# Kernel optimization log

Measured on AMD Instinct MI355X. Metric: run time of the kernel, lower is better.

The kernel has to match this reference:

```python
import jax, jax.numpy as jnp
import numpy as np

B, S, D = 2, 2048, 512
M = 64            # meta_memory_dim
C = 16            # n_chunks
H = 8             # attention heads
WIN = 512         # sliding window size
N_LAYERS = 2      # n_hidden_layers of ResLinear
MAX_ALR = 0.01    # max_adaptive_lr
LR, WD, EPS = 1e-3, 1e-2, 1e-8  # AdamW hyperparams (first step from zero state)
T = M + S


def lmm_apply(ws, x):
    # ResLinear: bias-free residual MLP blocks, x <- x + silu(x W^T)
    for W in ws:
        x = x + jax.nn.silu(x @ W.T)
    return x


def chunkify(t, c):
    # [B, T, D] -> [B, L, C, D] with contiguous chunks on axis 2 (vmap in_dims=2)
    b, t_, d = t.shape
    return jnp.moveaxis(t.reshape(b, c, t_ // c, d), 1, 2)


def swa(x, wq, wk, wv, wo):
    # causal sliding-window multi-head attention
    b, t, d = x.shape
    hd = d // H
    q = (x @ wq.T).reshape(b, t, H, hd)
    k = (x @ wk.T).reshape(b, t, H, hd)
    v = (x @ wv.T).reshape(b, t, H, hd)
    scores = jnp.einsum('bqhd,bkhd->bhqk', q, k) / jnp.sqrt(jnp.float32(hd))
    i = jnp.arange(t)[:, None]
    j = jnp.arange(t)[None, :]
    mask = (j <= i) & (i - j < WIN)
    scores = jnp.where(mask, scores, jnp.finfo(scores.dtype).min)
    attn = jax.nn.softmax(scores, axis=-1)
    out = jnp.einsum('bhqk,bkhd->bqhd', attn, v).reshape(b, t, d)
    return out @ wo.T


def setup_inputs() -> dict:
    key = jax.random.key(0)
    ks = jax.random.split(key, 11)
    sc = 0.02
    return {
        'x': jax.random.normal(ks[0], (B, S, D), jnp.float32),
        'meta_memory': jax.random.normal(ks[1], (M, D), jnp.float32),
        'lmm_w': jax.random.normal(ks[2], (N_LAYERS, D, D), jnp.float32) * sc,
        'w_q': jax.random.normal(ks[3], (D, D), jnp.float32) * sc,
        'w_k': jax.random.normal(ks[4], (D, D), jnp.float32) * sc,
        'w_v': jax.random.normal(ks[5], (D, D), jnp.float32) * sc,
        'w_lr': jax.random.normal(ks[6], (1, D), jnp.float32) * sc,
        'swa_wq': jax.random.normal(ks[7], (D, D), jnp.float32) * sc,
        'swa_wk': jax.random.normal(ks[8], (D, D), jnp.float32) * sc,
        'swa_wv': jax.random.normal(ks[9], (D, D), jnp.float32) * sc,
        'swa_wo': jax.random.normal(ks[10], (D, D), jnp.float32) * sc,
    }


def reference(x, meta_memory, lmm_w, w_q, w_k, w_v, w_lr, swa_wq, swa_wk, swa_wv, swa_wo):
    # inject meta memory tokens
    meta = jnp.broadcast_to(meta_memory, (x.shape[0],) + meta_memory.shape)
    xm = jnp.concatenate([meta, x], axis=1)                   # [B, T, D]

    queries = xm @ w_q.T                                      # [B, T, D] (n_chunks=1)
    keys = chunkify(xm @ w_k.T, C)                            # [B, L, C, D]
    values = chunkify(xm @ w_v.T, C)                          # [B, L, C, D]
    alr = chunkify(jax.nn.sigmoid(xm @ w_lr.T) * MAX_ALR, C)  # [B, L, C, 1]

    def assoc_loss(ws, k, v, w):
        preds = lmm_apply(ws, k)                              # [B, L, D]
        loss = jnp.mean((preds - v) ** 2, axis=-1)            # [B, L]
        return jnp.sum(loss * w[..., 0])

    # per-chunk test-time gradients of the associative loss
    grads = jax.vmap(jax.grad(assoc_loss), in_axes=(None, 2, 2, 2))(lmm_w, keys, values, alr)
    g = grads.mean(axis=0)                                    # [N_LAYERS, D, D]

    # first AdamW step from zero optimizer state: m_hat=g, v_hat=g^2
    lmm_w_new = lmm_w * (1.0 - LR * WD) - LR * g / (jnp.sqrt(g * g) + EPS)

    retrieved = lmm_apply(lmm_w_new, queries)                 # [B, T, D]
    retrieved = swa(retrieved, swa_wq, swa_wk, swa_wv, swa_wo)
    return retrieved[:, M:, :]                                # drop meta tokens
```

## Files before the change

### kernel.cpp

```cpp
#include <hip/hip_runtime.h>
#include <hip/hip_bf16.h>

#define B_   2
#define S_   2048
#define D_   512
#define M_   64
#define T_   2112
#define BT_  4224
#define H_   8
#define WIN_ 512

typedef short s16x8 __attribute__((ext_vector_type(8)));
typedef float f32x4 __attribute__((ext_vector_type(4)));
typedef unsigned short ushort_t;

__device__ __forceinline__ float siluf(float x) {
    float s = 1.0f / (1.0f + expf(-x));
    return x * s;
}
__device__ __forceinline__ float dsiluf(float x) {
    float s = 1.0f / (1.0f + expf(-x));
    return s * (1.0f + x * (1.0f - s));
}
__device__ __forceinline__ float bf2f(ushort_t u) {
    union { float f; unsigned int i; } x; x.i = ((unsigned int)u) << 16; return x.f;
}
__device__ __forceinline__ ushort_t f2bf(float f) {
    union { float f; unsigned int i; } x; x.f = f;
    unsigned int r = x.i + 0x7FFFu + ((x.i >> 16) & 1u);
    return (ushort_t)(r >> 16);
}
__device__ __forceinline__ void pack8(ushort_t* dst, const float* v) {
    ushort_t tmp[8];
#pragma unroll
    for (int i = 0; i < 8; ++i) tmp[i] = f2bf(v[i]);
    *(int4*)dst = *(const int4*)tmp;
}

__global__ void build_xm_kernel(const float* __restrict__ x, const float* __restrict__ meta,
                                ushort_t* __restrict__ xmb) {
    int idx = blockIdx.x * 256 + threadIdx.x;
    int seg = idx & 63;
    int row = idx >> 6;
    int b   = row / T_;
    int t   = row - b * T_;
    const float* src;
    if (t < M_) src = meta + (size_t)t * 512 + seg * 8;
    else        src = x + ((size_t)b * S_ + (t - M_)) * 512 + seg * 8;
    float v[8];
    *(float4*)&v[0] = *(const float4*)src;
    *(float4*)&v[4] = *(const float4*)(src + 4);
    pack8(xmb + (size_t)row * 512 + seg * 8, v);
}

struct W9 { const float* s[9]; ushort_t* d[9]; };
__global__ void cvt_w_kernel(W9 p) {
    int w = blockIdx.y;
    int idx = blockIdx.x * 256 + threadIdx.x;
    const float* src = p.s[w] + (size_t)idx * 8;
    float v[8];
    *(float4*)&v[0] = *(const float4*)src;
    *(float4*)&v[4] = *(const float4*)(src + 4);
    pack8(p.d[w] + (size_t)idx * 8, v);
}
__global__ void cvt_wT_kernel(const float* __restrict__ src, ushort_t* __restrict__ dst) {
    __shared__ float t[32][33];
    int tid = threadIdx.x;
    int tr = tid >> 3, tc = (tid & 7) * 4;
    int r0 = blockIdx.y * 32, c0 = blockIdx.x * 32;
    *(float4*)&t[tr][tc] = *(const float4*)&src[(size_t)(r0 + tr) * 512 + c0 + tc];
    __syncthreads();
    ushort_t o[4];
#pragma unroll
    for (int i = 0; i < 4; ++i) o[i] = f2bf(t[tc + i][tr]);
    *(ushort2*)&dst[(size_t)(c0 + tr) * 512 + r0 + tc] = *(ushort2*)&o[0];
    *(ushort2*)&dst[(size_t)(c0 + tr) * 512 + r0 + tc + 2] = *(ushort2*)&o[2];
}

__global__ void alr_kernel(const ushort_t* __restrict__ xmb, const float* __restrict__ wlr,
                           float* __restrict__ alr) {
    int r = blockIdx.x * 4 + (threadIdx.x >> 6);
    int lane = threadIdx.x & 63;
    const ushort_t* row = xmb + (size_t)r * D_;
    float s = 0.f;
#pragma unroll
    for (int k = 0; k < 8; ++k) s = fmaf(bf2f(row[lane + k * 64]), wlr[lane + k * 64], s);
#pragma unroll
    for (int off = 32; off >= 1; off >>= 1) s += __shfl_xor(s, off, 64);
    if (lane == 0) alr[r] = 0.01f / (1.0f + expf(-s));
}

template<int MODE>
__global__ __launch_bounds__(256)
void mgemm(const ushort_t* __restrict__ A, const ushort_t* __restrict__ Bt,
           float* __restrict__ F0, float* __restrict__ F1,
           ushort_t* __restrict__ U0, ushort_t* __restrict__ U1, ushort_t* __restrict__ U2,
           const float* __restrict__ alrp) {
    __shared__ ushort_t As[64 * 64];
    __shared__ ushort_t Bs[64 * 64];
    int tid = threadIdx.x;
    int m0 = blockIdx.x * 64, n0 = blockIdx.y * 64;
    int srow = tid >> 2;
    int sseg = (tid & 3) << 1;
    int wid = tid >> 6;
    int lane = tid & 63;
    int wm = (wid & 1) << 5;
    int wn = (wid >> 1) << 5;
    int fr = lane & 15;
    int fq = lane >> 4;
    f32x4 acc[2][2] = {};
    for (int k0 = 0; k0 < 512; k0 += 64) {
        const ushort_t* ga = A  + (size_t)(m0 + srow) * 512 + k0 + sseg * 8;
        const ushort_t* gb = Bt + (size_t)(n0 + srow) * 512 + k0 + sseg * 8;
        int4 av0 = *(const int4*)ga;
        int4 av1 = *(const int4*)(ga + 8);
        int4 bv0 = *(const int4*)gb;
        int4 bv1 = *(const int4*)(gb + 8);
        __syncthreads();
        int sw = srow & 7;
        *(int4*)&As[srow * 64 + ((sseg    ) ^ sw) * 8] = av0;
        *(int4*)&As[srow * 64 + ((sseg + 1) ^ sw) * 8] = av1;
        *(int4*)&Bs[srow * 64 + ((sseg    ) ^ sw) * 8] = bv0;
        *(int4*)&Bs[srow * 64 + ((sseg + 1) ^ sw) * 8] = bv1;
        __syncthreads();
#pragma unroll
        for (int ks = 0; ks < 2; ++ks) {
            int seg = fq + ks * 4;
            int rA0 = wm + fr,      rA1 = wm + 16 + fr;
            int rB0 = wn + fr,      rB1 = wn + 16 + fr;
            s16x8 a0 = *(const s16x8*)&As[rA0 * 64 + (seg ^ (rA0 & 7)) * 8];
            s16x8 a1 = *(const s16x8*)&As[rA1 * 64 + (seg ^ (rA1 & 7)) * 8];
            s16x8 b0 = *(const s16x8*)&Bs[rB0 * 64 + (seg ^ (rB0 & 7)) * 8];
            s16x8 b1 = *(const s16x8*)&Bs[rB1 * 64 + (seg ^ (rB1 & 7)) * 8];
            acc[0][0] = __builtin_amdgcn_mfma_f32_16x16x32_bf16(a0, b0, acc[0][0], 0, 0, 0);
            acc[0][1] = __builtin_amdgcn_mfma_f32_16x16x32_bf16(a0, b1, acc[0][1], 0, 0, 0);
            acc[1][0] = __builtin_amdgcn_mfma_f32_16x16x32_bf16(a1, b0, acc[1][0], 0, 0, 0);
            acc[1][1] = __builtin_amdgcn_mfma_f32_16x16x32_bf16(a1, b1, acc[1][1], 0, 0, 0);
        }
    }
#pragma unroll
    for (int i = 0; i < 2; ++i) {
        int row0 = m0 + wm + i * 16 + fq * 4;
        float c4[4];
        if (MODE == 2) {
#pragma unroll
            for (int r = 0; r < 4; ++r) c4[r] = (2.0f / 512.0f) * alrp[row0 + r];
        }
#pragma unroll
        for (int j = 0; j < 2; ++j) {
            int col = n0 + wn + j * 16 + fr;
            if (MODE == 0 || MODE == 5) {
                int sg = col >> 9;
                int cl = col & 511;
                if (MODE == 0) {
                    ushort_t* dst = (sg == 0) ? U0 : ((sg == 1) ? U1 : U2);
#pragma unroll
                    for (int r = 0; r < 4; ++r)
                        dst[(size_t)(row0 + r) * 512 + cl] = f2bf(acc[i][j][r]);
                } else {
                    if (sg == 0) {
#pragma unroll
                        for (int r = 0; r < 4; ++r)
                            U0[(size_t)(row0 + r) * 512 + cl] = f2bf(acc[i][j][r]);
                    } else if (sg == 1) {
#pragma unroll
                        for (int r = 0; r < 4; ++r)
                            U1[(size_t)(row0 + r) * 512 + cl] = f2bf(acc[i][j][r]);
                    } else {
                        int bb = row0 / T_;
                        int t0 = row0 - bb * T_;
                        ushort_t t4[4];
#pragma unroll
                        for (int r = 0; r < 4; ++r) t4[r] = f2bf(acc[i][j][r]);
                        *(uint2*)&U2[((size_t)(bb * 512) + cl) * T_ + t0] = *(uint2*)t4;
                    }
                }
            } else {
#pragma unroll
                for (int r = 0; r < 4; ++r) {
                    size_t off = (size_t)(row0 + r) * 512 + col;
                    float v = acc[i][j][r];
                    if (MODE == 1) {
                        F1[off] = v;
                        float h = bf2f(U1[off]) + siluf(v);
                        F0[off] = h;
                        U0[off] = f2bf(h);
                    } else if (MODE == 2) {
                        float z = v;
                        float s = 1.f / (1.f + expf(-z));
                        float d = c4[r] * (F0[off] + z * s - bf2f(U1[off]));
                        F1[off] = d;
                        U0[off] = f2bf(d * (s * (1.f + z * (1.f - s))));
                    } else if (MODE == 3) {
                        float g = F0[off] + v;
                        U0[off] = f2bf(g * dsiluf(F1[off]));
                    } else if (MODE == 4) {
                        U0[off] = f2bf(bf2f(U1[off]) + siluf(v));
                    } else if (MODE == 6) {
                        int row = row0 + r;
                        int bb = row / T_;
                        int t = row - bb * T_;
                        if (t >= M_) F0[((size_t)bb * S_ + (t - M_)) * 512 + col] = v;
                    }
                }
            }
        }
    }
}

__global__ __launch_bounds__(256)
void gemm_tn_bf(const ushort_t* __restrict__ A, const ushort_t* __restrict__ Bm,
                float* __restrict__ Cpart) {
    __shared__ ushort_t At[64 * 64];
    __shared__ ushort_t Bt[64 * 64];
    int tid = threadIdx.x;
    int m0 = blockIdx.x * 64, n0 = blockIdx.y * 64;
    int kbase = blockIdx.z * 704;
    int wave = tid >> 6, lane = tid & 63;
    int fr = lane & 15, fq = lane >> 4;
    int wm = (wave & 1) << 5, wn = (wave >> 1) << 5;
    int tok = tid & 63, cs0 = tid >> 6;
    f32x4 acc[2][2] = {};
    for (int kt = 0; kt < 11; ++kt) {
        int t0 = kbase + kt * 64;
        int4 av[2], bv[2];
#pragma unroll
        for (int p = 0; p < 2; ++p) {
            int cs = cs0 + p * 4;
            av[p] = *(const int4*)&A[(size_t)(t0 + tok) * 512 + m0 + cs * 8];
            bv[p] = *(const int4*)&Bm[(size_t)(t0 + tok) * 512 + n0 + cs * 8];
        }
        __syncthreads();
#pragma unroll
        for (int p = 0; p < 2; ++p) {
            int cs = cs0 + p * 4;
            const ushort_t* au = (const ushort_t*)&av[p];
            const ushort_t* bu = (const ushort_t*)&bv[p];
#pragma unroll
            for (int j = 0; j < 8; ++j) {
                int row = cs * 8 + j;
                At[row * 64 + (((tok >> 3) ^ j) << 3) + (tok & 7)] = au[j];
                Bt[row * 64 + (((tok >> 3) ^ j) << 3) + (tok & 7)] = bu[j];
            }
        }
        __syncthreads();
#pragma unroll
        for (int ks = 0; ks < 2; ++ks) {
            int seg = ks * 4 + fq;
            s16x8 a0 = *(const s16x8*)&At[(wm + fr) * 64      + ((seg ^ (fr & 7)) << 3)];
            s16x8 a1 = *(const s16x8*)&At[(wm + 16 + fr) * 64 + ((seg ^ (fr & 7)) << 3)];
            s16x8 b0 = *(const s16x8*)&Bt[(wn + fr) * 64      + ((seg ^ (fr & 7)) << 3)];
            s16x8 b1 = *(const s16x8*)&Bt[(wn + 16 + fr) * 64 + ((seg ^ (fr & 7)) << 3)];
            acc[0][0] = __builtin_amdgcn_mfma_f32_16x16x32_bf16(a0, b0, acc[0][0], 0, 0, 0);
            acc[0][1] = __builtin_amdgcn_mfma_f32_16x16x32_bf16(a0, b1, acc[0][1], 0, 0, 0);
            acc[1][0] = __builtin_amdgcn_mfma_f32_16x16x32_bf16(a1, b0, acc[1][0], 0, 0, 0);
            acc[1][1] = __builtin_amdgcn_mfma_f32_16x16x32_bf16(a1, b1, acc[1][1], 0, 0, 0);
        }
    }
    float* C = Cpart + (size_t)blockIdx.z * 262144;
#pragma unroll
    for (int i = 0; i < 2; ++i)
#pragma unroll
        for (int j = 0; j < 2; ++j)
#pragma unroll
            for (int r = 0; r < 4; ++r)
                C[(size_t)(m0 + wm + i * 16 + fq * 4 + r) * 512 + n0 + wn + j * 16 + fr] =
                    acc[i][j][r];
}

__global__ void adam_kernel(const float* __restrict__ W, const float* __restrict__ dWp,
                            ushort_t* __restrict__ Wnb) {
    int idx = blockIdx.x * 256 + threadIdx.x;
    int layer = idx >> 18;
    int i = idx & 262143;
    const float* base = dWp + (size_t)layer * 6 * 262144 + i;
    float g = 0.f;
#pragma unroll
    for (int z = 0; z < 6; ++z) g += base[(size_t)z * 262144];
    g *= (1.0f / 16.0f);
    float w = W[idx];
    float o = w * (1.0f - 1e-5f) - 1e-3f * g / (fabsf(g) + 1e-8f);
    Wnb[idx] = f2bf(o);
}

__global__ __launch_bounds__(256)
void swa_mfma(const ushort_t* __restrict__ qh, const ushort_t* __restrict__ kh,
              const ushort_t* __restrict__ vhT, ushort_t* __restrict__ ao) {
    __shared__ ushort_t Qs[64 * 64];
    __shared__ ushort_t Ks[64 * 64];
    __shared__ ushort_t Vs[64 * 64];
    __shared__ ushort_t Pw[4][16 * 72];
    int qt = 32 - (int)blockIdx.x;
    int hh = blockIdx.y;
    int b  = blockIdx.z;
    int tid = threadIdx.x;
    int wave = tid >> 6, lane = tid & 63;
    int fr = lane & 15, fq = lane >> 4;
    int tok = tid & 63, cs0 = tid >> 6;

    {
        const ushort_t* src = qh + ((size_t)(b * T_ + qt * 64 + tok)) * 512 + hh * 64;
#pragma unroll
        for (int p = 0; p < 2; ++p) {
            int seg = cs0 + p * 4;
            *(int4*)&Qs[tok * 64 + ((seg ^ (tok & 7)) << 3)] = *(const int4*)(src + seg * 8);
        }
    }
    __syncthreads();
    s16x8 qf0 = *(const s16x8*)&Qs[(wave * 16 + fr) * 64 + (((0 + fq) ^ (fr & 7)) << 3)];
    s16x8 qf1 = *(const s16x8*)&Qs[(wave * 16 + fr) * 64 + (((4 + fq) ^ (fr & 7)) << 3)];

    int i_q = qt * 64 + wave * 16 + fr;
    float m_i = -1e30f, l_i = 0.f;
    f32x4 o[4] = {};
    int jstart = qt * 64 - (WIN_ - 1);
    if (jstart < 0) jstart = 0;
    jstart &= ~63;
    for (int jb = jstart; jb <= qt * 64; jb += 64) {
        __syncthreads();
        {
            const ushort_t* ksrc = kh + ((size_t)(b * T_ + jb + tok)) * 512 + hh * 64;
            const ushort_t* vsrc = vhT + ((size_t)(b * 512 + hh * 64 + tok)) * T_ + jb;
#pragma unroll
            for (int p = 0; p < 2; ++p) {
                int seg = cs0 + p * 4;
                *(int4*)&Ks[tok * 64 + ((seg ^ (tok & 7)) << 3)] = *(const int4*)(ksrc + seg * 8);
                *(int4*)&Vs[tok * 64 + ((seg ^ (tok & 7)) << 3)] = *(const int4*)(vsrc + seg * 8);
            }
        }
        __syncthreads();
        f32x4 sa[4] = {};
#pragma unroll
        for (int kf = 0; kf < 4; ++kf) {
            int krow = kf * 16 + fr;
            s16x8 a0 = *(const s16x8*)&Ks[krow * 64 + (((0 + fq) ^ (fr & 7)) << 3)];
            s16x8 a1 = *(const s16x8*)&Ks[krow * 64 + (((4 + fq) ^ (fr & 7)) << 3)];
            sa[kf] = __builtin_amdgcn_mfma_f32_16x16x32_bf16(a0, qf0, sa[kf], 0, 0, 0);
            sa[kf] = __builtin_amdgcn_mfma_f32_16x16x32_bf16(a1, qf1, sa[kf], 0, 0, 0);
        }
        float sv[16];
        float tmax = -1e30f;
#pragma unroll
        for (int kf = 0; kf < 4; ++kf)
#pragma unroll
            for (int r = 0; r < 4; ++r) {
                int j2 = jb + kf * 16 + fq * 4 + r;
                bool valid = (j2 <= i_q) && (i_q - j2 < WIN_);
                float v = valid ? sa[kf][r] * 0.125f : -1e30f;
                sv[kf * 4 + r] = v;
                tmax = fmaxf(tmax, v);
            }
        tmax = fmaxf(tmax, __shfl_xor(tmax, 16));
        tmax = fmaxf(tmax, __shfl_xor(tmax, 32));
        float mn = fmaxf(m_i, tmax);
        float alpha = __expf(m_i - mn);
        m_i = mn;
        float psum = 0.f;
#pragma unroll
        for (int kf = 0; kf < 4; ++kf)
#pragma unroll
            for (int r = 0; r < 4; ++r) {
                float v = sv[kf * 4 + r];
                float p = (v > -1e29f) ? __expf(v - mn) : 0.f;
                ushort_t pb = f2bf(p);
                psum += bf2f(pb);
                Pw[wave][fr * 72 + kf * 16 + fq * 4 + r] = pb;
            }
        psum += __shfl_xor(psum, 16);
        psum += __shfl_xor(psum, 32);
        l_i = l_i * alpha + psum;
        float a0s = __shfl(alpha, fq * 4 + 0);
        float a1s = __shfl(alpha, fq * 4 + 1);
        float a2s = __shfl(alpha, fq * 4 + 2);
        float a3s = __shfl(alpha, fq * 4 + 3);
#pragma unroll
        for (int nf = 0; nf < 4; ++nf) {
            o[nf][0] *= a0s; o[nf][1] *= a1s; o[nf][2] *= a2s; o[nf][3] *= a3s;
        }
#pragma unroll
        for (int ks = 0; ks < 2; ++ks) {
            s16x8 pa = *(const s16x8*)&Pw[wave][fr * 72 + ks * 32 + fq * 8];
#pragma unroll
            for (int nf = 0; nf < 4; ++nf) {
                int vrow = nf * 16 + fr;
                s16x8 bv = *(const s16x8*)&Vs[vrow * 64 + (((ks * 4 + fq) ^ (fr & 7)) << 3)];
                o[nf] = __builtin_amdgcn_mfma_f32_16x16x32_bf16(pa, bv, o[nf], 0, 0, 0);
            }
        }
    }
    float linv = 1.0f / l_i;
    float l0 = __shfl(linv, fq * 4 + 0);
    float l1 = __shfl(linv, fq * 4 + 1);
    float l2 = __shfl(linv, fq * 4 + 2);
    float l3 = __shfl(linv, fq * 4 + 3);
#pragma unroll
    for (int nf = 0; nf < 4; ++nf) {
        int col = hh * 64 + nf * 16 + fr;
        size_t row0 = (size_t)(b * T_) + qt * 64 + wave * 16 + fq * 4;
        ao[(row0 + 0) * 512 + col] = f2bf(o[nf][0] * l0);
        ao[(row0 + 1) * 512 + col] = f2bf(o[nf][1] * l1);
        ao[(row0 + 2) * 512 + col] = f2bf(o[nf][2] * l2);
        ao[(row0 + 3) * 512 + col] = f2bf(o[nf][3] * l3);
    }
}

extern "C" void kernel_launch(void* const* d_in, const int* in_sizes, int n_in,
                              void* d_out, int out_size, void* d_ws, size_t ws_size,
                              hipStream_t stream) {
    (void)in_sizes; (void)n_in; (void)out_size; (void)ws_size;
    const float* x      = (const float*)d_in[0];
    const float* meta   = (const float*)d_in[1];
    const float* lmm_w  = (const float*)d_in[2];
    const float* w_q    = (const float*)d_in[3];
    const float* w_k    = (const float*)d_in[4];
    const float* w_v    = (const float*)d_in[5];
    const float* w_lr   = (const float*)d_in[6];
    const float* swa_wq = (const float*)d_in[7];
    const float* swa_wk = (const float*)d_in[8];
    const float* swa_wv = (const float*)d_in[9];
    const float* swa_wo = (const float*)d_in[10];
    float* out = (float*)d_out;
    float* ws  = (float*)d_ws;

    const size_t BTD = (size_t)BT_ * D_;
    float* b4 = ws + 0 * BTD;
    float* b5 = ws + 1 * BTD;
    float* b7 = ws + 2 * BTD;
    float* alr = ws + 3 * BTD;
    float* dWp = alr + BT_;
    ushort_t* xb = (ushort_t*)(dWp + 12 * 262144);
    ushort_t* xm_bf  = xb + 0 * BTD;
    ushort_t* qq_bf  = xb + 1 * BTD;
    ushort_t* kk_bf  = xb + 2 * BTD;
    ushort_t* vv_bf  = xb + 3 * BTD;
    ushort_t* h1_bf  = xb + 4 * BTD;
    ushort_t* dz1_bf = xb + 5 * BTD;
    ushort_t* r_bf   = xm_bf;
    ushort_t* h1q_bf = kk_bf;
    ushort_t* qh_bf  = qq_bf;
    ushort_t* kh_bf  = dz1_bf;
    ushort_t* dz0_bf = vv_bf;
    ushort_t* ao_bf  = vv_bf;
    ushort_t* vhT    = h1_bf;
    ushort_t* wbf = xb + 6 * BTD;
    ushort_t* wq_bf  = wbf + 0 * 262144;
    ushort_t* l0_bf  = wbf + 3 * 262144;
    ushort_t* l1_bf  = wbf + 4 * 262144;
    ushort_t* sq_bf  = wbf + 5 * 262144;
    ushort_t* wo_bf  = wbf + 8 * 262144;
    ushort_t* l1t_bf = wbf + 9 * 262144;
    ushort_t* wn_bf  = wbf + 10 * 262144;

    dim3 blk(256);
    dim3 g8(1056);
    dim3 gg(66, 8);
    dim3 gq(66, 24);
    dim3 gtn(8, 8, 6);

    W9 wl;
    wl.s[0] = w_q;    wl.d[0] = wq_bf;
    wl.s[1] = w_k;    wl.d[1] = wbf + 1 * 262144;
    wl.s[2] = w_v;    wl.d[2] = wbf + 2 * 262144;
    wl.s[3] = lmm_w;  wl.d[3] = l0_bf;
    wl.s[4] = lmm_w + 262144; wl.d[4] = l1_bf;
    wl.s[5] = swa_wq; wl.d[5] = sq_bf;
    wl.s[6] = swa_wk; wl.d[6] = wbf + 6 * 262144;
    wl.s[7] = swa_wv; wl.d[7] = wbf + 7 * 262144;
    wl.s[8] = swa_wo; wl.d[8] = wo_bf;

    cvt_w_kernel<<<dim3(128, 9), blk, 0, stream>>>(wl);
    cvt_wT_kernel<<<dim3(16, 16), blk, 0, stream>>>(lmm_w + 262144, l1t_bf);
    build_xm_kernel<<<g8, blk, 0, stream>>>(x, meta, xm_bf);
    alr_kernel<<<dim3(1056), blk, 0, stream>>>(xm_bf, w_lr, alr);
    mgemm<0><<<gq, blk, 0, stream>>>(xm_bf, wq_bf, nullptr, nullptr, qq_bf, kk_bf, vv_bf, nullptr);
    mgemm<1><<<gg, blk, 0, stream>>>(kk_bf, l0_bf, b5, b4, h1_bf, kk_bf, nullptr, nullptr);
    mgemm<2><<<gg, blk, 0, stream>>>(h1_bf, l1_bf, b5, b7, dz1_bf, vv_bf, nullptr, alr);
    mgemm<3><<<gg, blk, 0, stream>>>(dz1_bf, l1t_bf, b7, b4, dz0_bf, nullptr, nullptr, nullptr);
    gemm_tn_bf<<<gtn, blk, 0, stream>>>(dz1_bf, h1_bf, dWp + 6 * 262144);
    gemm_tn_bf<<<gtn, blk, 0, stream>>>(dz0_bf, kk_bf, dWp);
    adam_kernel<<<dim3(2048), blk, 0, stream>>>(lmm_w, dWp, wn_bf);
    mgemm<4><<<gg, blk, 0, stream>>>(qq_bf, wn_bf, nullptr, nullptr, h1q_bf, qq_bf, nullptr, nullptr);
    mgemm<4><<<gg, blk, 0, stream>>>(h1q_bf, wn_bf + 262144, nullptr, nullptr, r_bf, h1q_bf, nullptr, nullptr);
    mgemm<5><<<gq, blk, 0, stream>>>(r_bf, sq_bf, nullptr, nullptr, qh_bf, kh_bf, vhT, nullptr);
    swa_mfma<<<dim3(33, 8, 2), blk, 0, stream>>>(qh_bf, kh_bf, vhT, ao_bf);
    mgemm<6><<<gg, blk, 0, stream>>>(ao_bf, wo_bf, out, nullptr, nullptr, nullptr, nullptr, nullptr);
}
```

Before: 246.6 us.

## Fuse prep kernels, register-prefetch GEMM tiles, emit transposed operands for dW GEMMs

Merges the weight conversion, transpose, xm build and alr kernels into one prep launch, with alr now computed from fp32 inputs. Adds register prefetch of the next K tile in mgemm, the dW GEMM and the sliding-window attention loop, so global loads overlap the MFMA work. The forward GEMM epilogues now also write token-major transposed copies, which lets the dW GEMM load contiguous rows instead of scattering elements into shared memory. Attention skips mask evaluation for fully valid tiles. In exchange it needs more workspace buffers, more epilogue stores and more register pressure.

```diff
diff --git a/kernel.cpp b/kernel.cpp
--- a/kernel.cpp
+++ b/kernel.cpp
@@ -37,64 +37,72 @@
     *(int4*)dst = *(const int4*)tmp;
 }
 
-__global__ void build_xm_kernel(const float* __restrict__ x, const float* __restrict__ meta,
-                                ushort_t* __restrict__ xmb) {
-    int idx = blockIdx.x * 256 + threadIdx.x;
-    int seg = idx & 63;
-    int row = idx >> 6;
-    int b   = row / T_;
-    int t   = row - b * T_;
-    const float* src;
-    if (t < M_) src = meta + (size_t)t * 512 + seg * 8;
-    else        src = x + ((size_t)b * S_ + (t - M_)) * 512 + seg * 8;
-    float v[8];
-    *(float4*)&v[0] = *(const float4*)src;
-    *(float4*)&v[4] = *(const float4*)(src + 4);
-    pack8(xmb + (size_t)row * 512 + seg * 8, v);
-}
-
-struct W9 { const float* s[9]; ushort_t* d[9]; };
-__global__ void cvt_w_kernel(W9 p) {
-    int w = blockIdx.y;
-    int idx = blockIdx.x * 256 + threadIdx.x;
-    const float* src = p.s[w] + (size_t)idx * 8;
-    float v[8];
-    *(float4*)&v[0] = *(const float4*)src;
-    *(float4*)&v[4] = *(const float4*)(src + 4);
-    pack8(p.d[w] + (size_t)idx * 8, v);
-}
-__global__ void cvt_wT_kernel(const float* __restrict__ src, ushort_t* __restrict__ dst) {
-    __shared__ float t[32][33];
+struct PrepArgs {
+    const float* wsrc[9]; ushort_t* wdst[9];
+    const float* l1src;   ushort_t* l1t;
+    const float* x; const float* meta; ushort_t* xm;
+    const float* wlr; float* alr;
+};
+__global__ __launch_bounds__(256)
+void prep_kernel(PrepArgs p) {
+    __shared__ float tbuf[32][33];
+    int bid = blockIdx.x;
     int tid = threadIdx.x;
-    int tr = tid >> 3, tc = (tid & 7) * 4;
-    int r0 = blockIdx.y * 32, c0 = blockIdx.x * 32;
-    *(float4*)&t[tr][tc] = *(const float4*)&src[(size_t)(r0 + tr) * 512 + c0 + tc];
-    __syncthreads();
-    ushort_t o[4];
-#pragma unroll
-    for (int i = 0; i < 4; ++i) o[i] = f2bf(t[tc + i][tr]);
-    *(ushort2*)&dst[(size_t)(c0 + tr) * 512 + r0 + tc] = *(ushort2*)&o[0];
-    *(ushort2*)&dst[(size_t)(c0 + tr) * 512 + r0 + tc + 2] = *(ushort2*)&o[2];
-}
-
-__global__ void alr_kernel(const ushort_t* __restrict__ xmb, const float* __restrict__ wlr,
-                           float* __restrict__ alr) {
-    int r = blockIdx.x * 4 + (threadIdx.x >> 6);
-    int lane = threadIdx.x & 63;
-    const ushort_t* row = xmb + (size_t)r * D_;
-    float s = 0.f;
-#pragma unroll
-    for (int k = 0; k < 8; ++k) s = fmaf(bf2f(row[lane + k * 64]), wlr[lane + k * 64], s);
-#pragma unroll
-    for (int off = 32; off >= 1; off >>= 1) s += __shfl_xor(s, off, 64);
-    if (lane == 0) alr[r] = 0.01f / (1.0f + expf(-s));
+    if (bid < 1152) {
+        int w = bid >> 7;
+        int idx = ((bid & 127) << 8) + tid;
+        const float* src = p.wsrc[w] + (size_t)idx * 8;
+        float v[8];
+        *(float4*)&v[0] = *(const float4*)src;
+        *(float4*)&v[4] = *(const float4*)(src + 4);
+        pack8(p.wdst[w] + (size_t)idx * 8, v);
+    } else if (bid < 1408) {
+        int wz = bid - 1152;
+        int bx = wz & 15, by = wz >> 4;
+        int tr = tid >> 3, tc = (tid & 7) * 4;
+        int r0 = by * 32, c0 = bx * 32;
+        *(float4*)&tbuf[tr][tc] = *(const float4*)&p.l1src[(size_t)(r0 + tr) * 512 + c0 + tc];
+        __syncthreads();
+        ushort_t o[4];
+#pragma unroll
+        for (int i = 0; i < 4; ++i) o[i] = f2bf(tbuf[tc + i][tr]);
+        *(ushort2*)&p.l1t[(size_t)(c0 + tr) * 512 + r0 + tc] = *(ushort2*)&o[0];
+        *(ushort2*)&p.l1t[(size_t)(c0 + tr) * 512 + r0 + tc + 2] = *(ushort2*)&o[2];
+    } else if (bid < 2464) {
+        int idx = (bid - 1408) * 256 + tid;
+        int seg = idx & 63;
+        int row = idx >> 6;
+        int b = row / T_;
+        int t = row - b * T_;
+        const float* src;
+        if (t < M_) src = p.meta + (size_t)t * 512 + seg * 8;
+        else        src = p.x + ((size_t)b * S_ + (t - M_)) * 512 + seg * 8;
+        float v[8];
+        *(float4*)&v[0] = *(const float4*)src;
+        *(float4*)&v[4] = *(const float4*)(src + 4);
+        pack8(p.xm + (size_t)row * 512 + seg * 8, v);
+    } else {
+        int r = (bid - 2464) * 4 + (tid >> 6);
+        int lane = tid & 63;
+        int b = r / T_;
+        int t = r - b * T_;
+        const float* row = (t < M_) ? (p.meta + (size_t)t * 512)
+                                    : (p.x + ((size_t)b * S_ + (t - M_)) * 512);
+        float s = 0.f;
+#pragma unroll
+        for (int k = 0; k < 8; ++k) s = fmaf(row[lane + k * 64], p.wlr[lane + k * 64], s);
+#pragma unroll
+        for (int off = 32; off >= 1; off >>= 1) s += __shfl_xor(s, off, 64);
+        if (lane == 0) p.alr[r] = 0.01f / (1.0f + expf(-s));
+    }
 }
 
 template<int MODE>
 __global__ __launch_bounds__(256)
 void mgemm(const ushort_t* __restrict__ A, const ushort_t* __restrict__ Bt,
            float* __restrict__ F0, float* __restrict__ F1,
-           ushort_t* __restrict__ U0, ushort_t* __restrict__ U1, ushort_t* __restrict__ U2,
+           ushort_t* __restrict__ U0, ushort_t* __restrict__ U1,
+           ushort_t* __restrict__ U2, ushort_t* __restrict__ U3,
            const float* __restrict__ alrp) {
     __shared__ ushort_t As[64 * 64];
     __shared__ ushort_t Bs[64 * 64];
@@ -108,21 +116,27 @@
     int wn = (wid >> 1) << 5;
     int fr = lane & 15;
     int fq = lane >> 4;
+    int sw = srow & 7;
+    const ushort_t* ga = A  + (size_t)(m0 + srow) * 512 + sseg * 8;
+    const ushort_t* gb = Bt + (size_t)(n0 + srow) * 512 + sseg * 8;
+    int4 av0 = *(const int4*)ga;
+    int4 av1 = *(const int4*)(ga + 8);
+    int4 bv0 = *(const int4*)gb;
+    int4 bv1 = *(const int4*)(gb + 8);
     f32x4 acc[2][2] = {};
     for (int k0 = 0; k0 < 512; k0 += 64) {
-        const ushort_t* ga = A  + (size_t)(m0 + srow) * 512 + k0 + sseg * 8;
-        const ushort_t* gb = Bt + (size_t)(n0 + srow) * 512 + k0 + sseg * 8;
-        int4 av0 = *(const int4*)ga;
-        int4 av1 = *(const int4*)(ga + 8);
-        int4 bv0 = *(const int4*)gb;
-        int4 bv1 = *(const int4*)(gb + 8);
-        __syncthreads();
-        int sw = srow & 7;
+        __syncthreads();
         *(int4*)&As[srow * 64 + ((sseg    ) ^ sw) * 8] = av0;
         *(int4*)&As[srow * 64 + ((sseg + 1) ^ sw) * 8] = av1;
         *(int4*)&Bs[srow * 64 + ((sseg    ) ^ sw) * 8] = bv0;
         *(int4*)&Bs[srow * 64 + ((sseg + 1) ^ sw) * 8] = bv1;
         __syncthreads();
+        if (k0 + 64 < 512) {
+            av0 = *(const int4*)(ga + k0 + 64);
+            av1 = *(const int4*)(ga + k0 + 72);
+            bv0 = *(const int4*)(gb + k0 + 64);
+            bv1 = *(const int4*)(gb + k0 + 72);
+        }
 #pragma unroll
         for (int ks = 0; ks < 2; ++ks) {
             int seg = fq + ks * 4;
@@ -149,59 +163,88 @@
 #pragma unroll
         for (int j = 0; j < 2; ++j) {
             int col = n0 + wn + j * 16 + fr;
-            if (MODE == 0 || MODE == 5) {
-                int sg = col >> 9;
-                int cl = col & 511;
-                if (MODE == 0) {
-                    ushort_t* dst = (sg == 0) ? U0 : ((sg == 1) ? U1 : U2);
-#pragma unroll
-                    for (int r = 0; r < 4; ++r)
-                        dst[(size_t)(row0 + r) * 512 + cl] = f2bf(acc[i][j][r]);
+            if (MODE == 0) {
+                int sg = col >> 9, cl = col & 511;
+                ushort_t t4[4];
+#pragma unroll
+                for (int r = 0; r < 4; ++r) t4[r] = f2bf(acc[i][j][r]);
+                if (sg == 0) {
+#pragma unroll
+                    for (int r = 0; r < 4; ++r) U0[(size_t)(row0 + r) * 512 + cl] = t4[r];
+                } else if (sg == 1) {
+#pragma unroll
+                    for (int r = 0; r < 4; ++r) U1[(size_t)(row0 + r) * 512 + cl] = t4[r];
+                    *(uint2*)&U2[(size_t)cl * BT_ + row0] = *(uint2*)t4;
                 } else {
-                    if (sg == 0) {
-#pragma unroll
-                        for (int r = 0; r < 4; ++r)
-                            U0[(size_t)(row0 + r) * 512 + cl] = f2bf(acc[i][j][r]);
-                    } else if (sg == 1) {
-#pragma unroll
-                        for (int r = 0; r < 4; ++r)
-                            U1[(size_t)(row0 + r) * 512 + cl] = f2bf(acc[i][j][r]);
-                    } else {
-                        int bb = row0 / T_;
-                        int t0 = row0 - bb * T_;
-                        ushort_t t4[4];
-#pragma unroll
-                        for (int r = 0; r < 4; ++r) t4[r] = f2bf(acc[i][j][r]);
-                        *(uint2*)&U2[((size_t)(bb * 512) + cl) * T_ + t0] = *(uint2*)t4;
-                    }
-                }
-            } else {
+#pragma unroll
+                    for (int r = 0; r < 4; ++r) U3[(size_t)(row0 + r) * 512 + cl] = t4[r];
+                }
+            } else if (MODE == 5) {
+                int sg = col >> 9, cl = col & 511;
+                ushort_t t4[4];
+#pragma unroll
+                for (int r = 0; r < 4; ++r) t4[r] = f2bf(acc[i][j][r]);
+                if (sg == 0) {
+#pragma unroll
+                    for (int r = 0; r < 4; ++r) U0[(size_t)(row0 + r) * 512 + cl] = t4[r];
+                } else if (sg == 1) {
+#pragma unroll
+                    for (int r = 0; r < 4; ++r) U1[(size_t)(row0 + r) * 512 + cl] = t4[r];
+                } else {
+                    int bb = row0 / T_;
+                    int t0 = row0 - bb * T_;
+                    *(uint2*)&U2[((size_t)(bb * 512) + cl) * T_ + t0] = *(uint2*)t4;
+                }
+            } else if (MODE == 1) {
+                ushort_t t4[4];
 #pragma unroll
                 for (int r = 0; r < 4; ++r) {
                     size_t off = (size_t)(row0 + r) * 512 + col;
-                    float v = acc[i][j][r];
-                    if (MODE == 1) {
-                        F1[off] = v;
-                        float h = bf2f(U1[off]) + siluf(v);
-                        F0[off] = h;
-                        U0[off] = f2bf(h);
-                    } else if (MODE == 2) {
-                        float z = v;
-                        float s = 1.f / (1.f + expf(-z));
-                        float d = c4[r] * (F0[off] + z * s - bf2f(U1[off]));
-                        F1[off] = d;
-                        U0[off] = f2bf(d * (s * (1.f + z * (1.f - s))));
-                    } else if (MODE == 3) {
-                        float g = F0[off] + v;
-                        U0[off] = f2bf(g * dsiluf(F1[off]));
-                    } else if (MODE == 4) {
-                        U0[off] = f2bf(bf2f(U1[off]) + siluf(v));
-                    } else if (MODE == 6) {
-                        int row = row0 + r;
-                        int bb = row / T_;
-                        int t = row - bb * T_;
-                        if (t >= M_) F0[((size_t)bb * S_ + (t - M_)) * 512 + col] = v;
-                    }
+                    float z = acc[i][j][r];
+                    F1[off] = z;
+                    float h = bf2f(U1[off]) + siluf(z);
+                    F0[off] = h;
+                    ushort_t hb = f2bf(h);
+                    U0[off] = hb;
+                    t4[r] = hb;
+                }
+                *(uint2*)&U2[(size_t)col * BT_ + row0] = *(uint2*)t4;
+            } else if (MODE == 2) {
+                ushort_t t4[4];
+#pragma unroll
+                for (int r = 0; r < 4; ++r) {
+                    size_t off = (size_t)(row0 + r) * 512 + col;
+                    float z = acc[i][j][r];
+                    float s = 1.f / (1.f + expf(-z));
+                    float d = c4[r] * (F0[off] + z * s - bf2f(U1[off]));
+                    F1[off] = d;
+                    ushort_t u = f2bf(d * (s * (1.f + z * (1.f - s))));
+                    U0[off] = u;
+                    t4[r] = u;
+                }
+                *(uint2*)&U2[(size_t)col * BT_ + row0] = *(uint2*)t4;
+            } else if (MODE == 3) {
+                ushort_t t4[4];
+#pragma unroll
+                for (int r = 0; r < 4; ++r) {
+                    size_t off = (size_t)(row0 + r) * 512 + col;
+                    float g = F0[off] + acc[i][j][r];
+                    t4[r] = f2bf(g * dsiluf(F1[off]));
+                }
+                *(uint2*)&U0[(size_t)col * BT_ + row0] = *(uint2*)t4;
+            } else if (MODE == 4) {
+#pragma unroll
+                for (int r = 0; r < 4; ++r) {
+                    size_t off = (size_t)(row0 + r) * 512 + col;
+                    U0[off] = f2bf(bf2f(U1[off]) + siluf(acc[i][j][r]));
+                }
+            } else if (MODE == 6) {
+#pragma unroll
+                for (int r = 0; r < 4; ++r) {
+                    int row = row0 + r;
+                    int bb = row / T_;
+                    int t = row - bb * T_;
+                    if (t >= M_) F0[((size_t)bb * S_ + (t - M_)) * 512 + col] = acc[i][j][r];
                 }
             }
         }
@@ -209,48 +252,52 @@
 }
 
 __global__ __launch_bounds__(256)
-void gemm_tn_bf(const ushort_t* __restrict__ A, const ushort_t* __restrict__ Bm,
-                float* __restrict__ Cpart) {
-    __shared__ ushort_t At[64 * 64];
-    __shared__ ushort_t Bt[64 * 64];
+void gemm_dw(const ushort_t* __restrict__ AT, const ushort_t* __restrict__ BT2,
+             float* __restrict__ Cpart) {
+    __shared__ ushort_t As[64 * 64];
+    __shared__ ushort_t Bs[64 * 64];
     int tid = threadIdx.x;
     int m0 = blockIdx.x * 64, n0 = blockIdx.y * 64;
     int kbase = blockIdx.z * 704;
-    int wave = tid >> 6, lane = tid & 63;
-    int fr = lane & 15, fq = lane >> 4;
-    int wm = (wave & 1) << 5, wn = (wave >> 1) << 5;
-    int tok = tid & 63, cs0 = tid >> 6;
+    int srow = tid >> 2;
+    int sseg = (tid & 3) << 1;
+    int wid = tid >> 6;
+    int lane = tid & 63;
+    int wm = (wid & 1) << 5;
+    int wn = (wid >> 1) << 5;
+    int fr = lane & 15;
+    int fq = lane >> 4;
+    int sw = srow & 7;
+    const ushort_t* ga = AT  + (size_t)(m0 + srow) * BT_ + kbase + sseg * 8;
+    const ushort_t* gb = BT2 + (size_t)(n0 + srow) * BT_ + kbase + sseg * 8;
+    int4 av0 = *(const int4*)ga;
+    int4 av1 = *(const int4*)(ga + 8);
+    int4 bv0 = *(const int4*)gb;
+    int4 bv1 = *(const int4*)(gb + 8);
     f32x4 acc[2][2] = {};
     for (int kt = 0; kt < 11; ++kt) {
-        int t0 = kbase + kt * 64;
-        int4 av[2], bv[2];
-#pragma unroll
-        for (int p = 0; p < 2; ++p) {
-            int cs = cs0 + p * 4;
-            av[p] = *(const int4*)&A[(size_t)(t0 + tok) * 512 + m0 + cs * 8];
-            bv[p] = *(const int4*)&Bm[(size_t)(t0 + tok) * 512 + n0 + cs * 8];
-        }
-        __syncthreads();
-#pragma unroll
-        for (int p = 0; p < 2; ++p) {
-            int cs = cs0 + p * 4;
-            const ushort_t* au = (const ushort_t*)&av[p];
-            const ushort_t* bu = (const ushort_t*)&bv[p];
-#pragma unroll
-            for (int j = 0; j < 8; ++j) {
-                int row = cs * 8 + j;
-                At[row * 64 + (((tok >> 3) ^ j) << 3) + (tok & 7)] = au[j];
-                Bt[row * 64 + (((tok >> 3) ^ j) << 3) + (tok & 7)] = bu[j];
-            }
-        }
-        __syncthreads();
+        __syncthreads();
+        *(int4*)&As[srow * 64 + ((sseg    ) ^ sw) * 8] = av0;
+        *(int4*)&As[srow * 64 + ((sseg + 1) ^ sw) * 8] = av1;
+        *(int4*)&Bs[srow * 64 + ((sseg    ) ^ sw) * 8] = bv0;
+        *(int4*)&Bs[srow * 64 + ((sseg + 1) ^ sw) * 8] = bv1;
+        __syncthreads();
+        if (kt < 10) {
+            int koff = (kt + 1) * 64;
+            av0 = *(const int4*)(ga + koff);
+            av1 = *(const int4*)(ga + koff + 8);
+            bv0 = *(const int4*)(gb + koff);
+            bv1 = *(const int4*)(gb + koff + 8);
+        }
 #pragma unroll
         for (int ks = 0; ks < 2; ++ks) {
-            int seg = ks * 4 + fq;
-            s16x8 a0 = *(const s16x8*)&At[(wm + fr) * 64      + ((seg ^ (fr & 7)) << 3)];
-            s16x8 a1 = *(const s16x8*)&At[(wm + 16 + fr) * 64 + ((seg ^ (fr & 7)) << 3)];
-            s16x8 b0 = *(const s16x8*)&Bt[(wn + fr) * 64      + ((seg ^ (fr & 7)) << 3)];
-            s16x8 b1 = *(const s16x8*)&Bt[(wn + 16 + fr) * 64 + ((seg ^ (fr & 7)) << 3)];
+            int seg = fq + ks * 4;
+            int rA0 = wm + fr,      rA1 = wm + 16 + fr;
+            int rB0 = wn + fr,      rB1 = wn + 16 + fr;
+            s16x8 a0 = *(const s16x8*)&As[rA0 * 64 + (seg ^ (rA0 & 7)) * 8];
+            s16x8 a1 = *(const s16x8*)&As[rA1 * 64 + (seg ^ (rA1 & 7)) * 8];
+            s16x8 b0 = *(const s16x8*)&Bs[rB0 * 64 + (seg ^ (rB0 & 7)) * 8];
+            s16x8 b1 = *(const s16x8*)&Bs[rB1 * 64 + (seg ^ (rB1 & 7)) * 8];
             acc[0][0] = __builtin_amdgcn_mfma_f32_16x16x32_bf16(a0, b0, acc[0][0], 0, 0, 0);
             acc[0][1] = __builtin_amdgcn_mfma_f32_16x16x32_bf16(a0, b1, acc[0][1], 0, 0, 0);
             acc[1][0] = __builtin_amdgcn_mfma_f32_16x16x32_bf16(a1, b0, acc[1][0], 0, 0, 0);
@@ -311,24 +358,34 @@
     s16x8 qf1 = *(const s16x8*)&Qs[(wave * 16 + fr) * 64 + (((4 + fq) ^ (fr & 7)) << 3)];
 
     int i_q = qt * 64 + wave * 16 + fr;
+    int iqmin = qt * 64 + wave * 16;
     float m_i = -1e30f, l_i = 0.f;
     f32x4 o[4] = {};
     int jstart = qt * 64 - (WIN_ - 1);
     if (jstart < 0) jstart = 0;
     jstart &= ~63;
-    for (int jb = jstart; jb <= qt * 64; jb += 64) {
-        __syncthreads();
-        {
-            const ushort_t* ksrc = kh + ((size_t)(b * T_ + jb + tok)) * 512 + hh * 64;
-            const ushort_t* vsrc = vhT + ((size_t)(b * 512 + hh * 64 + tok)) * T_ + jb;
-#pragma unroll
-            for (int p = 0; p < 2; ++p) {
-                int seg = cs0 + p * 4;
-                *(int4*)&Ks[tok * 64 + ((seg ^ (tok & 7)) << 3)] = *(const int4*)(ksrc + seg * 8);
-                *(int4*)&Vs[tok * 64 + ((seg ^ (tok & 7)) << 3)] = *(const int4*)(vsrc + seg * 8);
-            }
-        }
-        __syncthreads();
+    int jend = qt * 64;
+    const ushort_t* kp = kh + ((size_t)(b * T_ + jstart + tok)) * 512 + hh * 64;
+    const ushort_t* vp = vhT + ((size_t)(b * 512 + hh * 64 + tok)) * T_ + jstart;
+    int4 ka = *(const int4*)(kp + cs0 * 8);
+    int4 kb2 = *(const int4*)(kp + (cs0 + 4) * 8);
+    int4 va = *(const int4*)(vp + cs0 * 8);
+    int4 vb2 = *(const int4*)(vp + (cs0 + 4) * 8);
+    for (int jb = jstart; jb <= jend; jb += 64) {
+        __syncthreads();
+        *(int4*)&Ks[tok * 64 + (((cs0    ) ^ (tok & 7)) << 3)] = ka;
+        *(int4*)&Ks[tok * 64 + (((cs0 + 4) ^ (tok & 7)) << 3)] = kb2;
+        *(int4*)&Vs[tok * 64 + (((cs0    ) ^ (tok & 7)) << 3)] = va;
+        *(int4*)&Vs[tok * 64 + (((cs0 + 4) ^ (tok & 7)) << 3)] = vb2;
+        __syncthreads();
+        if (jb + 64 <= jend) {
+            kp += 64 * 512;
+            vp += 64;
+            ka  = *(const int4*)(kp + cs0 * 8);
+            kb2 = *(const int4*)(kp + (cs0 + 4) * 8);
+            va  = *(const int4*)(vp + cs0 * 8);
+            vb2 = *(const int4*)(vp + (cs0 + 4) * 8);
+        }
         f32x4 sa[4] = {};
 #pragma unroll
         for (int kf = 0; kf < 4; ++kf) {
@@ -340,16 +397,28 @@
         }
         float sv[16];
         float tmax = -1e30f;
-#pragma unroll
-        for (int kf = 0; kf < 4; ++kf)
-#pragma unroll
-            for (int r = 0; r < 4; ++r) {
-                int j2 = jb + kf * 16 + fq * 4 + r;
-                bool valid = (j2 <= i_q) && (i_q - j2 < WIN_);
-                float v = valid ? sa[kf][r] * 0.125f : -1e30f;
-                sv[kf * 4 + r] = v;
-                tmax = fmaxf(tmax, v);
-            }
+        bool full = (jb + 63 <= iqmin) && (jb >= iqmin + 15 - (WIN_ - 1));
+        if (full) {
+#pragma unroll
+            for (int kf = 0; kf < 4; ++kf)
+#pragma unroll
+                for (int r = 0; r < 4; ++r) {
+                    float v = sa[kf][r] * 0.125f;
+                    sv[kf * 4 + r] = v;
+                    tmax = fmaxf(tmax, v);
+                }
+        } else {
+#pragma unroll
+            for (int kf = 0; kf < 4; ++kf)
+#pragma unroll
+                for (int r = 0; r < 4; ++r) {
+                    int j2 = jb + kf * 16 + fq * 4 + r;
+                    bool valid = (j2 <= i_q) && (i_q - j2 < WIN_);
+                    float v = valid ? sa[kf][r] * 0.125f : -1e30f;
+                    sv[kf * 4 + r] = v;
+                    tmax = fmaxf(tmax, v);
+                }
+        }
         tmax = fmaxf(tmax, __shfl_xor(tmax, 16));
         tmax = fmaxf(tmax, __shfl_xor(tmax, 32));
         float mn = fmaxf(m_i, tmax);
@@ -429,20 +498,16 @@
     float* alr = ws + 3 * BTD;
     float* dWp = alr + BT_;
     ushort_t* xb = (ushort_t*)(dWp + 12 * 262144);
-    ushort_t* xm_bf  = xb + 0 * BTD;
-    ushort_t* qq_bf  = xb + 1 * BTD;
-    ushort_t* kk_bf  = xb + 2 * BTD;
-    ushort_t* vv_bf  = xb + 3 * BTD;
-    ushort_t* h1_bf  = xb + 4 * BTD;
-    ushort_t* dz1_bf = xb + 5 * BTD;
-    ushort_t* r_bf   = xm_bf;
-    ushort_t* h1q_bf = kk_bf;
-    ushort_t* qh_bf  = qq_bf;
-    ushort_t* kh_bf  = dz1_bf;
-    ushort_t* dz0_bf = vv_bf;
-    ushort_t* ao_bf  = vv_bf;
-    ushort_t* vhT    = h1_bf;
-    ushort_t* wbf = xb + 6 * BTD;
+    ushort_t* B0 = xb + 0 * BTD;
+    ushort_t* B1 = xb + 1 * BTD;
+    ushort_t* B2 = xb + 2 * BTD;
+    ushort_t* B3 = xb + 3 * BTD;
+    ushort_t* B4 = xb + 4 * BTD;
+    ushort_t* B5 = xb + 5 * BTD;
+    ushort_t* B6 = xb + 6 * BTD;
+    ushort_t* B7 = xb + 7 * BTD;
+    ushort_t* B8 = xb + 8 * BTD;
+    ushort_t* wbf = xb + 9 * BTD;
     ushort_t* wq_bf  = wbf + 0 * 262144;
     ushort_t* l0_bf  = wbf + 3 * 262144;
     ushort_t* l1_bf  = wbf + 4 * 262144;
@@ -452,36 +517,35 @@
     ushort_t* wn_bf  = wbf + 10 * 262144;
 
     dim3 blk(256);
-    dim3 g8(1056);
     dim3 gg(66, 8);
     dim3 gq(66, 24);
-    dim3 gtn(8, 8, 6);
-
-    W9 wl;
-    wl.s[0] = w_q;    wl.d[0] = wq_bf;
-    wl.s[1] = w_k;    wl.d[1] = wbf + 1 * 262144;
-    wl.s[2] = w_v;    wl.d[2] = wbf + 2 * 262144;
-    wl.s[3] = lmm_w;  wl.d[3] = l0_bf;
-    wl.s[4] = lmm_w + 262144; wl.d[4] = l1_bf;
-    wl.s[5] = swa_wq; wl.d[5] = sq_bf;
-    wl.s[6] = swa_wk; wl.d[6] = wbf + 6 * 262144;
-    wl.s[7] = swa_wv; wl.d[7] = wbf + 7 * 262144;
-    wl.s[8] = swa_wo; wl.d[8] = wo_bf;
-
-    cvt_w_kernel<<<dim3(128, 9), blk, 0, stream>>>(wl);
-    cvt_wT_kernel<<<dim3(16, 16), blk, 0, stream>>>(lmm_w + 262144, l1t_bf);
-    build_xm_kernel<<<g8, blk, 0, stream>>>(x, meta, xm_bf);
-    alr_kernel<<<dim3(1056), blk, 0, stream>>>(xm_bf, w_lr, alr);
-    mgemm<0><<<gq, blk, 0, stream>>>(xm_bf, wq_bf, nullptr, nullptr, qq_bf, kk_bf, vv_bf, nullptr);
-    mgemm<1><<<gg, blk, 0, stream>>>(kk_bf, l0_bf, b5, b4, h1_bf, kk_bf, nullptr, nullptr);
-    mgemm<2><<<gg, blk, 0, stream>>>(h1_bf, l1_bf, b5, b7, dz1_bf, vv_bf, nullptr, alr);
-    mgemm<3><<<gg, blk, 0, stream>>>(dz1_bf, l1t_bf, b7, b4, dz0_bf, nullptr, nullptr, nullptr);
-    gemm_tn_bf<<<gtn, blk, 0, stream>>>(dz1_bf, h1_bf, dWp + 6 * 262144);
-    gemm_tn_bf<<<gtn, blk, 0, stream>>>(dz0_bf, kk_bf, dWp);
+    dim3 gdw(8, 8, 6);
+
+    PrepArgs pa;
+    pa.wsrc[0] = w_q;    pa.wdst[0] = wq_bf;
+    pa.wsrc[1] = w_k;    pa.wdst[1] = wbf + 1 * 262144;
+    pa.wsrc[2] = w_v;    pa.wdst[2] = wbf + 2 * 262144;
+    pa.wsrc[3] = lmm_w;  pa.wdst[3] = l0_bf;
+    pa.wsrc[4] = lmm_w + 262144; pa.wdst[4] = l1_bf;
+    pa.wsrc[5] = swa_wq; pa.wdst[5] = sq_bf;
+    pa.wsrc[6] = swa_wk; pa.wdst[6] = wbf + 6 * 262144;
+    pa.wsrc[7] = swa_wv; pa.wdst[7] = wbf + 7 * 262144;
+    pa.wsrc[8] = swa_wo; pa.wdst[8] = wo_bf;
+    pa.l1src = lmm_w + 262144; pa.l1t = l1t_bf;
+    pa.x = x; pa.meta = meta; pa.xm = B0;
+    pa.wlr = w_lr; pa.alr = alr;
+
+    prep_kernel<<<dim3(3520), blk, 0, stream>>>(pa);
+    mgemm<0><<<gq, blk, 0, stream>>>(B0, wq_bf, nullptr, nullptr, B1, B2, B3, B4, nullptr);
+    mgemm<1><<<gg, blk, 0, stream>>>(B2, l0_bf, b5, b4, B5, B2, B6, nullptr, nullptr);
+    mgemm<2><<<gg, blk, 0, stream>>>(B5, l1_bf, b5, b7, B7, B4, B8, nullptr, alr);
+    mgemm<3><<<gg, blk, 0, stream>>>(B7, l1t_bf, b7, b4, B0, nullptr, nullptr, nullptr, nullptr);
+    gemm_dw<<<gdw, blk, 0, stream>>>(B8, B6, dWp + 6 * 262144);
+    gemm_dw<<<gdw, blk, 0, stream>>>(B0, B3, dWp);
     adam_kernel<<<dim3(2048), blk, 0, stream>>>(lmm_w, dWp, wn_bf);
-    mgemm<4><<<gg, blk, 0, stream>>>(qq_bf, wn_bf, nullptr, nullptr, h1q_bf, qq_bf, nullptr, nullptr);
-    mgemm<4><<<gg, blk, 0, stream>>>(h1q_bf, wn_bf + 262144, nullptr, nullptr, r_bf, h1q_bf, nullptr, nullptr);
-    mgemm<5><<<gq, blk, 0, stream>>>(r_bf, sq_bf, nullptr, nullptr, qh_bf, kh_bf, vhT, nullptr);
-    swa_mfma<<<dim3(33, 8, 2), blk, 0, stream>>>(qh_bf, kh_bf, vhT, ao_bf);
-    mgemm<6><<<gg, blk, 0, stream>>>(ao_bf, wo_bf, out, nullptr, nullptr, nullptr, nullptr, nullptr);
-}
+    mgemm<4><<<gg, blk, 0, stream>>>(B1, wn_bf, nullptr, nullptr, B0, B1, nullptr, nullptr, nullptr);
+    mgemm<4><<<gg, blk, 0, stream>>>(B0, wn_bf + 262144, nullptr, nullptr, B4, B0, nullptr, nullptr, nullptr);
+    mgemm<5><<<gq, blk, 0, stream>>>(B4, sq_bf, nullptr, nullptr, B1, B5, B6, nullptr, nullptr);
+    swa_mfma<<<dim3(33, 8, 2), blk, 0, stream>>>(B1, B5, B6, B2);
+    mgemm<6><<<gg, blk, 0, stream>>>(B2, wo_bf, out, nullptr, nullptr, nullptr, nullptr, nullptr, nullptr);
+}
```

After: 217.6 us. 1.13x faster.
